# Kernel tuning notes

Measured on AMD Instinct MI355X. Metric: run time of the kernel, lower is better.

## Reference

```python
import jax, jax.numpy as jnp
import numpy as np

N = 50000    # nodes
E = 800000   # edges per block
D = 128      # embed_dim
H = 8        # heads
DH = D // H  # head dim
L = 2        # layers / blocks
IN = 128     # in_feats
P = 8192     # pos/neg pairs
FF = 2 * D   # FFN hidden
NEG_SLOPE = 0.2


def layer_norm(x, g, b, eps=1e-5):
    m = x.mean(-1, keepdims=True)
    v = ((x - m) ** 2).mean(-1, keepdims=True)
    return (x - m) / jnp.sqrt(v + eps) * g + b


def setup_inputs() -> dict:
    key = jax.random.key(0)
    ks = jax.random.split(key, 32)
    f32 = jnp.float32
    def w(k, shape, fan_in):
        return jax.random.normal(k, shape, f32) * (1.0 / np.sqrt(fan_in))
    inp = {
        'x': jax.random.normal(ks[0], (N, IN), f32),
        'src': jax.random.randint(ks[1], (L, E), 0, N),
        'dst': jax.random.randint(ks[2], (L, E), 0, N),
        'pos_src': jax.random.randint(ks[3], (P,), 0, N),
        'pos_dst': jax.random.randint(ks[4], (P,), 0, N),
        'neg_src': jax.random.randint(ks[5], (P,), 0, N),
        'neg_dst': jax.random.randint(ks[6], (P,), 0, N),
        # input projection
        'W_in': w(ks[7], (IN, D), IN), 'b_in': jnp.zeros((D,), f32),
        # per-layer attention weights, stacked over L
        'Wq': w(ks[8], (L, D, D), D), 'bq': jnp.zeros((L, D), f32),
        'Wk': w(ks[9], (L, D, D), D), 'bk': jnp.zeros((L, D), f32),
        'Wv': w(ks[10], (L, D, D), D), 'bv': jnp.zeros((L, D), f32),
        'Wo': w(ks[11], (L, D, D), D), 'bo': jnp.zeros((L, D), f32),
        'ln1_g': jnp.ones((L, D), f32), 'ln1_b': jnp.zeros((L, D), f32),
        'Wf1': w(ks[12], (L, D, FF), D), 'bf1': jnp.zeros((L, FF), f32),
        'Wf2': w(ks[13], (L, FF, D), FF), 'bf2': jnp.zeros((L, D), f32),
        'ln2_g': jnp.ones((L, D), f32), 'ln2_b': jnp.zeros((L, D), f32),
        # predictor MLP: D -> D//2 -> 1
        'Wp1': w(ks[14], (D, D // 2), D), 'bp1': jnp.zeros((D // 2,), f32),
        'Wp2': w(ks[15], (D // 2, 1), D // 2), 'bp2': jnp.zeros((1,), f32),
    }
    return inp


def reference(x, src, dst, pos_src, pos_dst, neg_src, neg_dst,
              W_in, b_in, Wq, bq, Wk, bk, Wv, bv, Wo, bo,
              ln1_g, ln1_b, Wf1, bf1, Wf2, bf2, ln2_g, ln2_b,
              Wp1, bp1, Wp2, bp2):
    scale = 1.0 / np.sqrt(DH)
    h = x @ W_in + b_in  # [N, D] (dropout is identity in eval mode)
    for l in range(L):
        s_l, d_l = src[l], dst[l]
        q = (h @ Wq[l] + bq[l]).reshape(N, H, DH)
        k = (h @ Wk[l] + bk[l]).reshape(N, H, DH)
        v = (h @ Wv[l] + bv[l]).reshape(N, H, DH)
        # per-edge attention scores [E, H]
        sc = jnp.einsum('ehd,ehd->eh', q[d_l], k[s_l]) * scale
        # segment softmax over incoming edges of each dst node
        m = jax.ops.segment_max(sc, d_l, num_segments=N)   # [N, H]
        ex = jnp.exp(sc - m[d_l])
        den = jax.ops.segment_sum(ex, d_l, num_segments=N)  # [N, H]
        alpha = ex / (den[d_l] + 1e-9)
        agg = jax.ops.segment_sum(alpha[..., None] * v[s_l], d_l,
                                  num_segments=N).reshape(N, D)
        h = layer_norm(h + agg @ Wo[l] + bo[l], ln1_g[l], ln1_b[l])
        ff = jax.nn.relu(h @ Wf1[l] + bf1[l]) @ Wf2[l] + bf2[l]
        h = layer_norm(h + ff, ln2_g[l], ln2_b[l])

    def predict(a, b):
        z = h[a] * h[b]  # gather-multiply edge scoring
        z = jax.nn.leaky_relu(z @ Wp1 + bp1, NEG_SLOPE)
        return z @ Wp2 + bp2  # [P, 1]

    pos_score = predict(pos_src, pos_dst)
    neg_score = predict(neg_src, neg_dst)
    return (pos_score, neg_score, h)
```

## Files before the change

kernel.cpp:

```cpp
#include <hip/hip_runtime.h>
#include <hip/hip_bf16.h>
#include <math.h>

#define N_NODES 50000
#define NE      800000
#define D       128
#define H       8
#define DH      16
#define NLAYER  2
#define IN_F    128
#define PP      8192
#define FF      256
#define MPAD    50048
#define CAP     96
#define NBIN    196
#define BCAP    48
#define GCAP    4608
#define CHUNK   2048

typedef short  bf16x8 __attribute__((ext_vector_type(8)));
typedef float  f32x4  __attribute__((ext_vector_type(4)));
typedef __hip_bfloat16 bf16;
typedef unsigned short u16;
typedef unsigned int   u32;

__device__ __forceinline__ float bflo(u32 u) { return __uint_as_float(u << 16); }
__device__ __forceinline__ float bfhi(u32 u) { return __uint_as_float(u & 0xffff0000u); }

__global__ __launch_bounds__(256) void bin_kernel(
    const int* __restrict__ dst, const int* __restrict__ src,
    u32* __restrict__ gbin, int* __restrict__ gbin_cnt)
{
    __shared__ u32 ent[NBIN * BCAP];
    __shared__ int bcnt[NBIN];
    const int t = threadIdx.x, l = blockIdx.y;
    const int base = blockIdx.x * CHUNK;
    if (t < NBIN) bcnt[t] = 0;
    __syncthreads();
    #pragma unroll
    for (int j = 0; j < CHUNK / 256; j++) {
        int e = base + j * 256 + t;
        if (e < NE) {
            int d = dst[(size_t)l * NE + e];
            int s = src[(size_t)l * NE + e];
            int bin = d >> 8;
            int slot = atomicAdd(&bcnt[bin], 1);
            if (slot < BCAP) ent[bin * BCAP + slot] = ((u32)s << 16) | (u32)(d & 255);
        }
    }
    __syncthreads();
    if (t < NBIN) {
        int c = bcnt[t]; if (c > BCAP) c = BCAP;
        if (c > 0) {
            int gb = atomicAdd(&gbin_cnt[l * NBIN + t], c);
            u32* gp = gbin + ((size_t)l * NBIN + t) * GCAP;
            for (int i = 0; i < c; i++)
                if (gb + i < GCAP) gp[gb + i] = ent[t * BCAP + i];
        }
    }
}

__global__ __launch_bounds__(256) void expand_kernel(
    const u32* __restrict__ gbin, const int* __restrict__ gbin_cnt,
    int* __restrict__ cnt, u16* __restrict__ ssrc)
{
    __shared__ int lcnt[256];
    const int t = threadIdx.x, b = blockIdx.x, l = blockIdx.y;
    lcnt[t] = 0;
    __syncthreads();
    int n = gbin_cnt[l * NBIN + b]; if (n > GCAP) n = GCAP;
    const u32* gp = gbin + ((size_t)l * NBIN + b) * GCAP;
    for (int i = t; i < n; i += 256) {
        u32 u = gp[i];
        int dl = (int)(u & 255);
        int pos = atomicAdd(&lcnt[dl], 1);
        if (pos < CAP) {
            int d = (b << 8) + dl;
            ssrc[((size_t)l * N_NODES + d) * CAP + pos] = (u16)(u >> 16);
        }
    }
    __syncthreads();
    int d = (b << 8) + t;
    if (d < N_NODES) cnt[l * N_NODES + d] = lcnt[t];
}

__global__ void xb_kernel(const float* __restrict__ x, bf16* __restrict__ xb) {
    int id = blockIdx.x * blockDim.x + threadIdx.x;
    if (id >= MPAD * IN_F) return;
    int r = id / IN_F;
    xb[id] = __float2bfloat16(r < N_NODES ? x[id] : 0.f);
}

__global__ void prep_kernel(const float* __restrict__ W_in,
                            const float* __restrict__ Wq, const float* __restrict__ Wk,
                            const float* __restrict__ Wv, const float* __restrict__ Wo,
                            const float* __restrict__ Wf1, const float* __restrict__ Wf2,
                            const float* __restrict__ bq, const float* __restrict__ bk,
                            const float* __restrict__ bv,
                            bf16* __restrict__ win_t, bf16* __restrict__ wqkv_t,
                            bf16* __restrict__ wo_t, bf16* __restrict__ wf1_t,
                            bf16* __restrict__ wf2_t, float* __restrict__ bqkv)
{
    int id = blockIdx.x * blockDim.x + threadIdx.x;
    if (id < 16384) {
        int n = id >> 7, k = id & 127;
        win_t[id] = __float2bfloat16(W_in[k * 128 + n]);
        return;
    }
    id -= 16384;
    if (id < NLAYER * 49152) {
        int l = id / 49152, j = id % 49152;
        int r = j >> 7, k = j & 127;
        const float* Ws; int col;
        if (r < 128) { Ws = Wq; col = r; }
        else {
            int u = r - 128, hh = u >> 5, w = u & 31;
            if (w < 16) { Ws = Wk; col = hh * 16 + w; }
            else        { Ws = Wv; col = hh * 16 + w - 16; }
        }
        wqkv_t[(size_t)l * 49152 + j] = __float2bfloat16(Ws[(size_t)l * 16384 + k * 128 + col]);
        return;
    }
    id -= NLAYER * 49152;
    if (id < NLAYER * 16384) {
        int l = id / 16384, j = id % 16384;
        int n = j >> 7, k = j & 127;
        wo_t[id] = __float2bfloat16(Wo[(size_t)l * 16384 + k * 128 + n]);
        return;
    }
    id -= NLAYER * 16384;
    if (id < NLAYER * 32768) {
        int l = id / 32768, j = id % 32768;
        int n = j >> 7, k = j & 127;
        wf1_t[id] = __float2bfloat16(Wf1[(size_t)l * 32768 + k * 256 + n]);
        return;
    }
    id -= NLAYER * 32768;
    if (id < NLAYER * 32768) {
        int l = id / 32768, j = id % 32768;
        int n = j >> 8, k = j & 255;
        wf2_t[id] = __float2bfloat16(Wf2[(size_t)l * 32768 + k * 128 + n]);
        return;
    }
    id -= NLAYER * 32768;
    if (id < NLAYER * 384) {
        int l = id / 384, r = id % 384;
        float v;
        if (r < 128) v = bq[l * 128 + r];
        else {
            int u = r - 128, hh = u >> 5, w = u & 31;
            v = (w < 16) ? bk[l * 128 + hh * 16 + w] : bv[l * 128 + hh * 16 + w - 16];
        }
        bqkv[l * 384 + r] = v;
    }
}

__global__ __launch_bounds__(256) void gemm_mfma(
    const bf16* __restrict__ A, const bf16* __restrict__ Wt,
    const float* __restrict__ bias,
    float* __restrict__ Cf, bf16* __restrict__ Cb,
    int Mvalid, int K, int Nc, int lda, int relu)
{
    __shared__ float4 As4[1024];
    __shared__ float4 Bs4[1024];
    char* As = (char*)As4;
    char* Bs = (char*)Bs4;
    const int t = threadIdx.x;
    const int wave = t >> 6, lane = t & 63;
    const int wr = wave >> 1, wc = wave & 1;
    const int r0 = blockIdx.x * 128, c0 = blockIdx.y * 128;

    f32x4 acc[4][4] = {};

    const int lrow   = t >> 3;
    const int lcol16 = (t & 7) * 16;

    for (int k0 = 0; k0 < K; k0 += 64) {
        #pragma unroll
        for (int p = 0; p < 4; p++) {
            int row = p * 32 + lrow;
            float4 av = *(const float4*)((const char*)(A  + (size_t)(r0 + row) * lda + k0) + lcol16);
            float4 bv = *(const float4*)((const char*)(Wt + (size_t)(c0 + row) * K + k0) + lcol16);
            int sw = lcol16 ^ ((row & 7) << 4);
            *(float4*)(As + row * 128 + sw) = av;
            *(float4*)(Bs + row * 128 + sw) = bv;
        }
        __syncthreads();
        #pragma unroll
        for (int kk = 0; kk < 2; kk++) {
            bf16x8 af[4], bfr[4];
            int kbyte = kk * 64 + (lane >> 4) * 16;
            #pragma unroll
            for (int m = 0; m < 4; m++) {
                int rowa = wr * 64 + m * 16 + (lane & 15);
                af[m]  = *(const bf16x8*)(As + rowa * 128 + (kbyte ^ ((rowa & 7) << 4)));
                int rowb = wc * 64 + m * 16 + (lane & 15);
                bfr[m] = *(const bf16x8*)(Bs + rowb * 128 + (kbyte ^ ((rowb & 7) << 4)));
            }
            #pragma unroll
            for (int m = 0; m < 4; m++)
                #pragma unroll
                for (int n = 0; n < 4; n++)
                    acc[m][n] = __builtin_amdgcn_mfma_f32_16x16x32_bf16(af[m], bfr[n], acc[m][n], 0, 0, 0);
        }
        __syncthreads();
    }

    const int colbase = c0 + wc * 64 + (lane & 15);
    const int rowbase = r0 + wr * 64 + ((lane >> 4) << 2);
    #pragma unroll
    for (int n = 0; n < 4; n++) {
        int col = colbase + n * 16;
        float bsv = bias[col];
        #pragma unroll
        for (int m = 0; m < 4; m++) {
            #pragma unroll
            for (int i = 0; i < 4; i++) {
                int row = rowbase + m * 16 + i;
                if (row < Mvalid) {
                    float v = acc[m][n][i] + bsv;
                    if (relu) v = fmaxf(v, 0.f);
                    if (Cf) Cf[(size_t)row * Nc + col] = v;
                    if (Cb) Cb[(size_t)row * Nc + col] = __float2bfloat16(v);
                }
            }
        }
    }
}

__global__ __launch_bounds__(256) void gemm_ln(
    const bf16* __restrict__ A, const bf16* __restrict__ Wt,
    const float* __restrict__ bias, const float* __restrict__ g,
    const float* __restrict__ be,
    float* __restrict__ h, bf16* __restrict__ hb,
    int K, int lda)
{
    __shared__ float4 As4[512];
    __shared__ float4 Bs4[1024];
    char* As = (char*)As4;
    char* Bs = (char*)Bs4;
    const int t = threadIdx.x;
    const int w = t >> 6, lane = t & 63;
    const int r0 = blockIdx.x * 64;

    f32x4 acc[8] = {};

    for (int k0 = 0; k0 < K; k0 += 64) {
        {
            int row = t >> 2;
            int c16 = (t & 3) * 32;
            const char* ap = (const char*)(A + (size_t)(r0 + row) * lda + k0);
            float4 a0 = *(const float4*)(ap + c16);
            float4 a1 = *(const float4*)(ap + c16 + 16);
            *(float4*)(As + row * 128 + ((c16)      ^ ((row & 7) << 4))) = a0;
            *(float4*)(As + row * 128 + ((c16 + 16) ^ ((row & 7) << 4))) = a1;
        }
        {
            int row = t >> 1;
            int c16 = (t & 1) * 64;
            const char* bp = (const char*)(Wt + (size_t)row * K + k0);
            #pragma unroll
            for (int j = 0; j < 4; j++) {
                float4 b = *(const float4*)(bp + c16 + j * 16);
                *(float4*)(Bs + row * 128 + ((c16 + j * 16) ^ ((row & 7) << 4))) = b;
            }
        }
        __syncthreads();
        #pragma unroll
        for (int kk = 0; kk < 2; kk++) {
            int kbyte = kk * 64 + (lane >> 4) * 16;
            int rowa = w * 16 + (lane & 15);
            bf16x8 af = *(const bf16x8*)(As + rowa * 128 + (kbyte ^ ((rowa & 7) << 4)));
            #pragma unroll
            for (int n = 0; n < 8; n++) {
                int rowb = n * 16 + (lane & 15);
                bf16x8 bf8 = *(const bf16x8*)(Bs + rowb * 128 + (kbyte ^ ((rowb & 7) << 4)));
                acc[n] = __builtin_amdgcn_mfma_f32_16x16x32_bf16(af, bf8, acc[n], 0, 0, 0);
            }
        }
        __syncthreads();
    }

    const int sub = lane >> 4;
    const int c   = lane & 15;
    float bsv[8], gv[8], bev[8];
    #pragma unroll
    for (int n = 0; n < 8; n++) {
        int col = n * 16 + c;
        bsv[n] = bias[col]; gv[n] = g[col]; bev[n] = be[col];
    }
    #pragma unroll
    for (int i = 0; i < 4; i++) {
        int row = r0 + w * 16 + sub * 4 + i;
        bool ok = row < N_NODES;
        float x[8];
        float s = 0.f;
        #pragma unroll
        for (int n = 0; n < 8; n++) {
            float res = ok ? h[(size_t)row * D + n * 16 + c] : 0.f;
            x[n] = res + acc[n][i] + bsv[n];
            s += x[n];
        }
        s += __shfl_xor(s, 1); s += __shfl_xor(s, 2);
        s += __shfl_xor(s, 4); s += __shfl_xor(s, 8);
        float mean = s * (1.f / 128.f);
        float v = 0.f;
        #pragma unroll
        for (int n = 0; n < 8; n++) { float dd = x[n] - mean; v += dd * dd; }
        v += __shfl_xor(v, 1); v += __shfl_xor(v, 2);
        v += __shfl_xor(v, 4); v += __shfl_xor(v, 8);
        float rstd = rsqrtf(v * (1.f / 128.f) + 1e-5f);
        if (ok) {
            #pragma unroll
            for (int n = 0; n < 8; n++) {
                float o = (x[n] - mean) * rstd * gv[n] + bev[n];
                h [(size_t)row * D + n * 16 + c] = o;
                hb[(size_t)row * D + n * 16 + c] = __float2bfloat16(o);
            }
        }
    }
}

__global__ __launch_bounds__(256) void attn_fused(
    const bf16* __restrict__ qkv,
    const int* __restrict__ cnt, const u16* __restrict__ ssrc,
    bf16* __restrict__ aggout)
{
    const float S2 = 0.25f * 1.44269504088896f;
    int wid = threadIdx.x >> 6, lane = threadIdx.x & 63;
    int d = blockIdx.x * 4 + wid;
    if (d >= N_NODES) return;
    int slot = lane >> 3, h = lane & 7;

    const u32* qr = (const u32*)(qkv + (size_t)d * 384 + h * DH);
    float qf[16];
    {
        uint4 q0 = *(const uint4*)(qr);
        uint4 q1 = *(const uint4*)(qr + 4);
        qf[0]=bflo(q0.x); qf[1]=bfhi(q0.x); qf[2]=bflo(q0.y); qf[3]=bfhi(q0.y);
        qf[4]=bflo(q0.z); qf[5]=bfhi(q0.z); qf[6]=bflo(q0.w); qf[7]=bfhi(q0.w);
        qf[8]=bflo(q1.x); qf[9]=bfhi(q1.x); qf[10]=bflo(q1.y); qf[11]=bfhi(q1.y);
        qf[12]=bflo(q1.z); qf[13]=bfhi(q1.z); qf[14]=bflo(q1.w); qf[15]=bfhi(q1.w);
    }

    int deg = cnt[d];
    if (deg > CAP) deg = CAP;
    const u16* bp = ssrc + (size_t)d * CAP;
    float m2 = -INFINITY, den = 0.f;
    float acc[16] = {};

    for (int i = slot; i < deg; i += 8) {
        int s = bp[i];
        const uint4* kvp = (const uint4*)(qkv + (size_t)s * 384 + 128 + h * 32);
        uint4 k0 = kvp[0], k1 = kvp[1], v0 = kvp[2], v1 = kvp[3];
        float p = qf[0]*bflo(k0.x) + qf[1]*bfhi(k0.x)
                + qf[2]*bflo(k0.y) + qf[3]*bfhi(k0.y)
                + qf[4]*bflo(k0.z) + qf[5]*bfhi(k0.z)
                + qf[6]*bflo(k0.w) + qf[7]*bfhi(k0.w)
                + qf[8]*bflo(k1.x) + qf[9]*bfhi(k1.x)
                + qf[10]*bflo(k1.y) + qf[11]*bfhi(k1.y)
                + qf[12]*bflo(k1.z) + qf[13]*bfhi(k1.z)
                + qf[14]*bflo(k1.w) + qf[15]*bfhi(k1.w);
        float p2 = p * S2;
        float w;
        if (p2 > m2 + 8.f) {
            float f = exp2f(m2 - p2);
            den *= f;
            #pragma unroll
            for (int j = 0; j < 16; j++) acc[j] *= f;
            m2 = p2;
            w = 1.f;
        } else {
            w = exp2f(p2 - m2);
        }
        den += w;
        acc[0]  += w*bflo(v0.x); acc[1]  += w*bfhi(v0.x);
        acc[2]  += w*bflo(v0.y); acc[3]  += w*bfhi(v0.y);
        acc[4]  += w*bflo(v0.z); acc[5]  += w*bfhi(v0.z);
        acc[6]  += w*bflo(v0.w); acc[7]  += w*bfhi(v0.w);
        acc[8]  += w*bflo(v1.x); acc[9]  += w*bfhi(v1.x);
        acc[10] += w*bflo(v1.y); acc[11] += w*bfhi(v1.y);
        acc[12] += w*bflo(v1.z); acc[13] += w*bfhi(v1.z);
        acc[14] += w*bflo(v1.w); acc[15] += w*bfhi(v1.w);
    }

    #pragma unroll
    for (int o = 8; o < 64; o <<= 1) {
        float om   = __shfl_xor(m2, o);
        float oden = __shfl_xor(den, o);
        float M = fmaxf(m2, om);
        float fa = (m2 > -INFINITY) ? exp2f(m2 - M) : 0.f;
        float fb = (om > -INFINITY) ? exp2f(om - M) : 0.f;
        den = den * fa + oden * fb;
        #pragma unroll
        for (int j = 0; j < 16; j++) {
            float oa = __shfl_xor(acc[j], o);
            acc[j] = acc[j] * fa + oa * fb;
        }
        m2 = M;
    }

    float r = 1.f / (den + 1e-9f);
    float o0 = 0.f, o1 = 0.f;
    #pragma unroll
    for (int j = 0; j < 8; j++) {
        if (slot == j) { o0 = acc[2 * j]; o1 = acc[2 * j + 1]; }
    }
    bf16* op = aggout + (size_t)d * 384 + h * DH + slot * 2;
    op[0] = __float2bfloat16(o0 * r);
    op[1] = __float2bfloat16(o1 * r);
}

__global__ void predict_kernel(const float* __restrict__ h,
                               const int* __restrict__ ps, const int* __restrict__ pd,
                               const int* __restrict__ ns, const int* __restrict__ nd,
                               const float* __restrict__ Wp1, const float* __restrict__ bp1,
                               const float* __restrict__ Wp2, const float* __restrict__ bp2,
                               float* __restrict__ out)
{
    __shared__ float z[128];
    int p = blockIdx.x;
    int a, b;
    if (p < PP) { a = ps[p]; b = pd[p]; }
    else        { a = ns[p - PP]; b = nd[p - PP]; }
    int t = threadIdx.x;
    z[t]      = h[(size_t)a * D + t]      * h[(size_t)b * D + t];
    z[t + 64] = h[(size_t)a * D + t + 64] * h[(size_t)b * D + t + 64];
    __syncthreads();
    float acc = bp1[t];
    #pragma unroll 4
    for (int i = 0; i < 128; i++) acc += z[i] * Wp1[(size_t)i * 64 + t];
    acc = acc > 0.f ? acc : 0.2f * acc;
    float part = acc * Wp2[t];
    #pragma unroll
    for (int o = 32; o > 0; o >>= 1) part += __shfl_down(part, o);
    if (t == 0) out[p] = part + bp2[0];
}

extern "C" void kernel_launch(void* const* d_in, const int* in_sizes, int n_in,
                              void* d_out, int out_size, void* d_ws, size_t ws_size,
                              hipStream_t stream)
{
    const float* x       = (const float*)d_in[0];
    const int*   src     = (const int*)d_in[1];
    const int*   dst     = (const int*)d_in[2];
    const int*   pos_src = (const int*)d_in[3];
    const int*   pos_dst = (const int*)d_in[4];
    const int*   neg_src = (const int*)d_in[5];
    const int*   neg_dst = (const int*)d_in[6];
    const float* W_in = (const float*)d_in[7];
    const float* b_in = (const float*)d_in[8];
    const float* Wq = (const float*)d_in[9];
    const float* bq = (const float*)d_in[10];
    const float* Wk = (const float*)d_in[11];
    const float* bk = (const float*)d_in[12];
    const float* Wv = (const float*)d_in[13];
    const float* bv = (const float*)d_in[14];
    const float* Wo = (const float*)d_in[15];
    const float* bo = (const float*)d_in[16];
    const float* ln1g = (const float*)d_in[17];
    const float* ln1b = (const float*)d_in[18];
    const float* Wf1 = (const float*)d_in[19];
    const float* bf1 = (const float*)d_in[20];
    const float* Wf2 = (const float*)d_in[21];
    const float* bf2 = (const float*)d_in[22];
    const float* ln2g = (const float*)d_in[23];
    const float* ln2b = (const float*)d_in[24];
    const float* Wp1 = (const float*)d_in[25];
    const float* bp1 = (const float*)d_in[26];
    const float* Wp2 = (const float*)d_in[27];
    const float* bp2 = (const float*)d_in[28];

    float* out = (float*)d_out;
    float* h   = out + 2 * PP;

    bf16* B    = (bf16*)d_ws;
    bf16* qkvb = B;
    bf16* xb   = B;
    bf16* ffb  = B;
    bf16* hb   = B + (size_t)MPAD * 384;
    int*  cnt  = (int*)(hb + (size_t)MPAD * 128);
    u16*  ssrc = (u16*)(cnt + 2 * N_NODES);
    bf16* wtb  = (bf16*)(ssrc + (size_t)2 * N_NODES * CAP);
    bf16* win_t  = wtb;
    bf16* wqkv_t = wtb + 16384;
    bf16* wo_t   = wtb + 16384 + 98304;
    bf16* wf1_t  = wtb + 16384 + 98304 + 32768;
    bf16* wf2_t  = wtb + 16384 + 98304 + 32768 + 65536;
    float* bqkv  = (float*)(wtb + 16384 + 98304 + 32768 + 65536 + 65536);
    int*  gbin_cnt = (int*)(bqkv + NLAYER * 384);
    u32*  gbin     = (u32*)(gbin_cnt + 2 * NBIN);

    auto cdiv = [](int a, int b) { return (a + b - 1) / b; };
    const int GX = MPAD / 128;
    const int GL = MPAD / 64;

    xb_kernel<<<cdiv(MPAD * IN_F, 256), 256, 0, stream>>>(x, xb);
    prep_kernel<<<1091, 256, 0, stream>>>(W_in, Wq, Wk, Wv, Wo, Wf1, Wf2, bq, bk, bv,
                                          win_t, wqkv_t, wo_t, wf1_t, wf2_t, bqkv);

    hipMemsetAsync(gbin_cnt, 0, 2 * NBIN * sizeof(int), stream);
    bin_kernel<<<dim3(cdiv(NE, CHUNK), 2), 256, 0, stream>>>(dst, src, gbin, gbin_cnt);
    expand_kernel<<<dim3(NBIN, 2), 256, 0, stream>>>(gbin, gbin_cnt, cnt, ssrc);

    gemm_mfma<<<dim3(GX, 1), 256, 0, stream>>>(xb, win_t, b_in, h, hb, N_NODES, 128, 128, 128, 0);

    for (int l = 0; l < NLAYER; l++) {
        gemm_mfma<<<dim3(GX, 3), 256, 0, stream>>>(hb, wqkv_t + l * 49152, bqkv + l * 384,
                                                   nullptr, qkvb, N_NODES, 128, 384, 128, 0);

        attn_fused<<<cdiv(N_NODES, 4), 256, 0, stream>>>(qkvb, cnt + l * N_NODES,
                                                         ssrc + (size_t)l * N_NODES * CAP, qkvb);

        gemm_ln<<<GL, 256, 0, stream>>>(qkvb, wo_t + l * 16384, bo + l * D,
                                        ln1g + l * D, ln1b + l * D, h, hb, 128, 384);

        gemm_mfma<<<dim3(GX, 2), 256, 0, stream>>>(hb, wf1_t + l * 32768, bf1 + l * FF,
                                                   nullptr, ffb, N_NODES, 128, 256, 128, 1);
        gemm_ln<<<GL, 256, 0, stream>>>(ffb, wf2_t + l * 32768, bf2 + l * D,
                                        ln2g + l * D, ln2b + l * D, h, hb, 256, 256);
    }

    predict_kernel<<<2 * PP, 64, 0, stream>>>(h, pos_src, pos_dst, neg_src, neg_dst,
                                              Wp1, bp1, Wp2, bp2, out);
}
```

Before: 404.3 us.

## Fuse FFN up-projection, ReLU, down-projection and LayerNorm into one kernel

Replaces the separate FF1 GEMM and FF2 GEMM+LayerNorm launches with one kernel per 64-row tile. The ReLU hidden activations stay in LDS as bf16 instead of being written to and read back from a global buffer. This removes one launch and the round trip of a 50k x 256 bf16 intermediate per layer. In exchange it uses 80KB of LDS per block, which lowers occupancy, and it reloads the weight chunks into LDS in every block with a sync after each load.

```diff
diff --git a/kernel.cpp b/kernel.cpp
--- a/kernel.cpp
+++ b/kernel.cpp
@@ -299,6 +299,146 @@
         for (int n = 0; n < 8; n++) {
             float res = ok ? h[(size_t)row * D + n * 16 + c] : 0.f;
             x[n] = res + acc[n][i] + bsv[n];
+            s += x[n];
+        }
+        s += __shfl_xor(s, 1); s += __shfl_xor(s, 2);
+        s += __shfl_xor(s, 4); s += __shfl_xor(s, 8);
+        float mean = s * (1.f / 128.f);
+        float v = 0.f;
+        #pragma unroll
+        for (int n = 0; n < 8; n++) { float dd = x[n] - mean; v += dd * dd; }
+        v += __shfl_xor(v, 1); v += __shfl_xor(v, 2);
+        v += __shfl_xor(v, 4); v += __shfl_xor(v, 8);
+        float rstd = rsqrtf(v * (1.f / 128.f) + 1e-5f);
+        if (ok) {
+            #pragma unroll
+            for (int n = 0; n < 8; n++) {
+                float o = (x[n] - mean) * rstd * gv[n] + bev[n];
+                h [(size_t)row * D + n * 16 + c] = o;
+                hb[(size_t)row * D + n * 16 + c] = __float2bfloat16(o);
+            }
+        }
+    }
+}
+
+__global__ __launch_bounds__(256) void ffn_fused(
+    const bf16* __restrict__ A,
+    const bf16* __restrict__ Wf1t,
+    const float* __restrict__ b1,
+    const bf16* __restrict__ Wf2t,
+    const float* __restrict__ b2,
+    const float* __restrict__ g, const float* __restrict__ be,
+    float* __restrict__ h, bf16* __restrict__ hb)
+{
+    __shared__ char lds[81920];
+    char* As = lds;
+    char* Xs = lds + 16384;
+    char* Bs = lds + 49152;
+    const int t = threadIdx.x;
+    const int w = t >> 6, lane = t & 63;
+    const int r0 = blockIdx.x * 64;
+    const int c = lane & 15, sub = lane >> 4;
+
+    {
+        int row = t >> 2;
+        int off = (t & 3) * 64;
+        const char* ap = (const char*)(A + (size_t)(r0 + row) * 128);
+        #pragma unroll
+        for (int j = 0; j < 4; j++) {
+            float4 v = *(const float4*)(ap + off + j * 16);
+            *(float4*)(As + row * 256 + ((off + j * 16) ^ ((row & 7) << 4))) = v;
+        }
+    }
+
+    f32x4 acc1[16] = {};
+    #pragma unroll
+    for (int kc = 0; kc < 2; kc++) {
+        {
+            int row = t;
+            const char* bp = (const char*)Wf1t + row * 256 + kc * 128;
+            #pragma unroll
+            for (int j = 0; j < 8; j++) {
+                float4 v = *(const float4*)(bp + j * 16);
+                *(float4*)(Bs + row * 128 + ((j * 16) ^ ((row & 7) << 4))) = v;
+            }
+        }
+        __syncthreads();
+        #pragma unroll
+        for (int kkl = 0; kkl < 2; kkl++) {
+            int abyte = (kc * 2 + kkl) * 64 + sub * 16;
+            int rowa = w * 16 + c;
+            bf16x8 af = *(const bf16x8*)(As + rowa * 256 + (abyte ^ ((rowa & 7) << 4)));
+            int bbyte = kkl * 64 + sub * 16;
+            #pragma unroll
+            for (int n = 0; n < 16; n++) {
+                int rowb = n * 16 + c;
+                bf16x8 bf8 = *(const bf16x8*)(Bs + rowb * 128 + (bbyte ^ ((rowb & 7) << 4)));
+                acc1[n] = __builtin_amdgcn_mfma_f32_16x16x32_bf16(af, bf8, acc1[n], 0, 0, 0);
+            }
+        }
+        __syncthreads();
+    }
+
+    #pragma unroll
+    for (int n = 0; n < 16; n++) {
+        float bs = b1[n * 16 + c];
+        #pragma unroll
+        for (int i = 0; i < 4; i++) {
+            int row = w * 16 + sub * 4 + i;
+            float v = fmaxf(acc1[n][i] + bs, 0.f);
+            int byte = (n * 16 + c) * 2;
+            int addr = row * 512 + ((byte & ~15) ^ ((row & 7) << 4)) + (byte & 15);
+            *(bf16*)(Xs + addr) = __float2bfloat16(v);
+        }
+    }
+    __syncthreads();
+
+    f32x4 acc2[8] = {};
+    #pragma unroll
+    for (int kc = 0; kc < 2; kc++) {
+        {
+            int row = t >> 1;
+            int off = (t & 1) * 128;
+            const char* bp = (const char*)Wf2t + row * 512 + kc * 256 + off;
+            #pragma unroll
+            for (int j = 0; j < 8; j++) {
+                float4 v = *(const float4*)(bp + j * 16);
+                *(float4*)(Bs + row * 256 + ((off + j * 16) ^ ((row & 7) << 4))) = v;
+            }
+        }
+        __syncthreads();
+        #pragma unroll
+        for (int kkl = 0; kkl < 4; kkl++) {
+            int xbyte = kc * 256 + kkl * 64 + sub * 16;
+            int rowa = w * 16 + c;
+            bf16x8 af = *(const bf16x8*)(Xs + rowa * 512 + (xbyte ^ ((rowa & 7) << 4)));
+            int bbyte = kkl * 64 + sub * 16;
+            #pragma unroll
+            for (int n = 0; n < 8; n++) {
+                int rowb = n * 16 + c;
+                bf16x8 bf8 = *(const bf16x8*)(Bs + rowb * 256 + (bbyte ^ ((rowb & 7) << 4)));
+                acc2[n] = __builtin_amdgcn_mfma_f32_16x16x32_bf16(af, bf8, acc2[n], 0, 0, 0);
+            }
+        }
+        __syncthreads();
+    }
+
+    float bsv[8], gv[8], bev[8];
+    #pragma unroll
+    for (int n = 0; n < 8; n++) {
+        int col = n * 16 + c;
+        bsv[n] = b2[col]; gv[n] = g[col]; bev[n] = be[col];
+    }
+    #pragma unroll
+    for (int i = 0; i < 4; i++) {
+        int row = r0 + w * 16 + sub * 4 + i;
+        bool ok = row < N_NODES;
+        float x[8];
+        float s = 0.f;
+        #pragma unroll
+        for (int n = 0; n < 8; n++) {
+            float res = ok ? h[(size_t)row * D + n * 16 + c] : 0.f;
+            x[n] = res + acc2[n][i] + bsv[n];
             s += x[n];
         }
         s += __shfl_xor(s, 1); s += __shfl_xor(s, 2);
@@ -477,7 +617,6 @@
     bf16* B    = (bf16*)d_ws;
     bf16* qkvb = B;
     bf16* xb   = B;
-    bf16* ffb  = B;
     bf16* hb   = B + (size_t)MPAD * 384;
     int*  cnt  = (int*)(hb + (size_t)MPAD * 128);
     u16*  ssrc = (u16*)(cnt + 2 * N_NODES);
@@ -499,7 +638,7 @@
     prep_kernel<<<1091, 256, 0, stream>>>(W_in, Wq, Wk, Wv, Wo, Wf1, Wf2, bq, bk, bv,
                                           win_t, wqkv_t, wo_t, wf1_t, wf2_t, bqkv);
 
-    hipMemsetAsync(gbin_cnt, 0, 2 * NBIN * sizeof(int), stream);
+    (void)hipMemsetAsync(gbin_cnt, 0, 2 * NBIN * sizeof(int), stream);
     bin_kernel<<<dim3(cdiv(NE, CHUNK), 2), 256, 0, stream>>>(dst, src, gbin, gbin_cnt);
     expand_kernel<<<dim3(NBIN, 2), 256, 0, stream>>>(gbin, gbin_cnt, cnt, ssrc);
 
@@ -515,10 +654,9 @@
         gemm_ln<<<GL, 256, 0, stream>>>(qkvb, wo_t + l * 16384, bo + l * D,
                                         ln1g + l * D, ln1b + l * D, h, hb, 128, 384);
 
-        gemm_mfma<<<dim3(GX, 2), 256, 0, stream>>>(hb, wf1_t + l * 32768, bf1 + l * FF,
-                                                   nullptr, ffb, N_NODES, 128, 256, 128, 1);
-        gemm_ln<<<GL, 256, 0, stream>>>(ffb, wf2_t + l * 32768, bf2 + l * D,
-                                        ln2g + l * D, ln2b + l * D, h, hb, 256, 256);
+        ffn_fused<<<GL, 256, 0, stream>>>(hb, wf1_t + l * 32768, bf1 + l * FF,
+                                          wf2_t + l * 32768, bf2 + l * D,
+                                          ln2g + l * D, ln2b + l * D, h, hb);
     }
 
     predict_kernel<<<2 * PP, 64, 0, stream>>>(h, pos_src, pos_dst, neg_src, neg_dst,
```

Measured after the change: 377.8 us. 6.5% less time.
